# Kernel optimization log

Measured on AMD Instinct MI355X. Metric: run time of the kernel, lower is better.

## Reference

```python
import jax, jax.numpy as jnp
import numpy as np

I, H, L, B, T, EH = 256, 512, 2, 64, 2048, 128

def _leaky(x):
    return jnp.where(x > 0, x, 0.01 * x)

def _alpha(x):
    p = jax.nn.sigmoid(x)
    return p / (1.0 - p)

def _encoder(x, w1, b1, w2, b2, w3, b3):
    x = _leaky(x @ w1.T + b1)
    x = _leaky(x @ w2.T + b2)
    return _alpha(x @ w3.T + b3)

def setup_inputs() -> dict:
    key = jax.random.key(0)
    ks = jax.random.split(key, 24)
    def w(k, shape, fan_in):
        return jax.random.uniform(k, shape, jnp.float32, -1.0, 1.0) / np.sqrt(fan_in)
    inp = {
        "input": jax.random.normal(ks[0], (B, T, I), jnp.float32),
        "h0": jnp.zeros((L, B, H), jnp.float32),
        "c0": jnp.zeros((L, B, H), jnp.float32),
        # LSTM layer 0
        "W_ih0": w(ks[1], (4 * H, I), H), "W_hh0": w(ks[2], (4 * H, H), H),
        "b_ih0": w(ks[3], (4 * H,), H), "b_hh0": w(ks[4], (4 * H,), H),
        # LSTM layer 1
        "W_ih1": w(ks[5], (4 * H, H), H), "W_hh1": w(ks[6], (4 * H, H), H),
        "b_ih1": w(ks[7], (4 * H,), H), "b_hh1": w(ks[8], (4 * H,), H),
        # posterior_y encoder (input_size -> 128 -> 128 -> input_size)
        "ey_w1": w(ks[9], (EH, I), I), "ey_b1": w(ks[10], (EH,), I),
        "ey_w2": w(ks[11], (EH, EH), EH), "ey_b2": w(ks[12], (EH,), EH),
        "ey_w3": w(ks[13], (I, EH), EH), "ey_b3": w(ks[14], (I,), EH),
        # posterior_h encoder (hidden_size -> 128 -> 128 -> hidden_size)
        "eh_w1": w(ks[15], (EH, H), H), "eh_b1": w(ks[16], (EH,), H),
        "eh_w2": w(ks[17], (EH, EH), EH), "eh_b2": w(ks[18], (EH,), EH),
        "eh_w3": w(ks[19], (H, EH), EH), "eh_b3": w(ks[20], (H,), EH),
    }
    return inp

def reference(input, h0, c0,
              W_ih0, W_hh0, b_ih0, b_hh0,
              W_ih1, W_hh1, b_ih1, b_hh1,
              ey_w1, ey_b1, ey_w2, ey_b2, ey_w3, ey_b3,
              eh_w1, eh_b1, eh_w2, eh_b2, eh_w3, eh_b3):
    W_ih = [W_ih0, W_ih1]; W_hh = [W_hh0, W_hh1]
    b_ih = [b_ih0, b_ih1]; b_hh = [b_hh0, b_hh1]

    def step(carry, x_t):  # x_t: [B, I]
        h, c = carry  # each [L, B, H]
        alpha_y = _encoder(x_t, ey_w1, ey_b1, ey_w2, ey_b2, ey_w3, ey_b3)
        alpha_h = _encoder(h, eh_w1, eh_b1, eh_w2, eh_b2, eh_w3, eh_b3)
        h = h * alpha_h          # eval mode: noise = 1.0
        x = x_t * alpha_y
        new_h, new_c = [], []
        for l in range(L):
            gates = x @ W_ih[l].T + b_ih[l] + h[l] @ W_hh[l].T + b_hh[l]
            i, f, g, o = jnp.split(gates, 4, axis=-1)
            c_l = jax.nn.sigmoid(f) * c[l] + jax.nn.sigmoid(i) * jnp.tanh(g)
            h_l = jax.nn.sigmoid(o) * jnp.tanh(c_l)
            new_h.append(h_l); new_c.append(c_l)
            x = h_l
        return (jnp.stack(new_h), jnp.stack(new_c)), x  # x = top-layer h

    (h_n, c_n), ys = jax.lax.scan(step, (h0, c0), jnp.swapaxes(input, 0, 1))
    outputs = jnp.swapaxes(ys, 0, 1)  # [B, T, H]
    return outputs, h_n, c_n
```

## Files before the change

kernel.cpp:

```cpp
#include <hip/hip_runtime.h>
#include <math.h>
#include <stdint.h>

#define TT 2048
#define BB 64
#define II 256
#define HH 512
#define EHD 128
#define NGATE 64
#define NWG 68

typedef __attribute__((ext_vector_type(8))) short s16x8;
typedef __attribute__((ext_vector_type(4))) float f32x4;
typedef __attribute__((ext_vector_type(4))) uint32_t u32x4;

#define WAITVM(N) asm volatile("s_waitcnt vmcnt(" #N ")" ::: "memory")
#define VMFENCE() do { asm volatile("" ::: "memory"); __builtin_amdgcn_sched_barrier(0); } while(0)

__device__ __forceinline__ float dot4(const float4 a, const float4 b){
    return a.x*b.x + a.y*b.y + a.z*b.z + a.w*b.w;
}
__device__ __forceinline__ float sigm(float x){ return 1.0f/(1.0f+expf(-x)); }
__device__ __forceinline__ float leakyf(float x){ return x > 0.0f ? x : 0.01f*x; }
__device__ __forceinline__ float alphaf(float x){
    float p = 1.0f/(1.0f+expf(-x));
    return p/(1.0f-p);
}
__device__ __forceinline__ f32x4 MFMA(s16x8 a, s16x8 b, f32x4 c){
    return __builtin_amdgcn_mfma_f32_16x16x32_bf16(a, b, c, 0, 0, 0);
}

__device__ __forceinline__ uint32_t cld_u32(const uint32_t* p){
    return __hip_atomic_load(p, __ATOMIC_RELAXED, __HIP_MEMORY_SCOPE_AGENT);
}
__device__ __forceinline__ uint64_t cld_u64(const uint64_t* p){
    return __hip_atomic_load(p, __ATOMIC_RELAXED, __HIP_MEMORY_SCOPE_AGENT);
}
__device__ __forceinline__ void cst_u32(uint32_t* p, uint32_t v){
    __hip_atomic_store(p, v, __ATOMIC_RELAXED, __HIP_MEMORY_SCOPE_AGENT);
}

__device__ __forceinline__ uint32_t packsplit(float v){
    uint32_t u  = __float_as_uint(v);
    uint32_t hi = u & 0xFFFF0000u;
    float    lo = v - __uint_as_float(hi);
    return hi | (__float_as_uint(lo) >> 16);
}
__device__ __forceinline__ float unpackf(uint32_t w){
    return __uint_as_float(w & 0xFFFF0000u) + __uint_as_float(w << 16);
}

__device__ __forceinline__ void stage16(const void* g, void* l){
    __builtin_amdgcn_global_load_lds(
        (const __attribute__((address_space(1))) void*)g,
        (__attribute__((address_space(3))) void*)l, 16, 0, 0);
}

__device__ __forceinline__ void gbar(int* bar, int target){
    asm volatile("s_waitcnt vmcnt(0)" ::: "memory");
    __syncthreads();
    if (threadIdx.x == 0){
        __hip_atomic_fetch_add(bar, 1, __ATOMIC_RELAXED, __HIP_MEMORY_SCOPE_AGENT);
        while (__hip_atomic_load(bar, __ATOMIC_RELAXED, __HIP_MEMORY_SCOPE_AGENT) < target)
            __builtin_amdgcn_s_sleep(1);
    }
    __syncthreads();
}

__device__ __forceinline__ void wgbar(){ __builtin_amdgcn_s_barrier(); }
__device__ __forceinline__ void wgbar_lgkm(){
    asm volatile("s_waitcnt lgkmcnt(0)" ::: "memory");
    __builtin_amdgcn_s_barrier();
}

__device__ __forceinline__ void mk_frag(const uint64_t d[4], s16x8* hi, s16x8* lo){
    union { u32x4 u; s16x8 s; } H, L;
    #pragma unroll
    for (int i = 0; i < 4; i++){
        uint32_t x0 = (uint32_t)d[i], x1 = (uint32_t)(d[i] >> 32);
        H.u[i] = __builtin_amdgcn_perm(x1, x0, 0x07060302u);
        L.u[i] = __builtin_amdgcn_perm(x1, x0, 0x05040100u);
    }
    *hi = H.s; *lo = L.s;
}
__device__ __forceinline__ void pack8(const float* f, s16x8* hi, s16x8* lo){
    union { u32x4 u; s16x8 s; } H, L;
    #pragma unroll
    for (int i = 0; i < 4; i++){
        float a = f[2*i], b = f[2*i+1];
        uint32_t ua = __float_as_uint(a), ub = __float_as_uint(b);
        uint32_t ha = ua & 0xFFFF0000u, hb = ub & 0xFFFF0000u;
        H.u[i] = (ua >> 16) | hb;
        float la = a - __uint_as_float(ha), lb = b - __uint_as_float(hb);
        L.u[i] = (__float_as_uint(la) >> 16) | (__float_as_uint(lb) & 0xFFFF0000u);
    }
    *hi = H.s; *lo = L.s;
}

__device__ void enc_h_block(int e, const uint32_t* __restrict__ hsrc,
                            uint32_t* __restrict__ htil,
                            const float* __restrict__ w1, const float* __restrict__ b1,
                            const float* __restrict__ w2, const float* __restrict__ b2,
                            const float* __restrict__ w3, const float* __restrict__ b3,
                            float* smem)
{
    float* hlds = smem;
    float* t1   = smem + 4*516;
    float* t2   = t1 + 4*132;
    const int tid = threadIdx.x;
    const int r0 = e * 4;
    #pragma unroll
    for (int i = 0; i < 8; i++){
        int el = tid + i*256;
        int rr = el >> 9, k = el & 511;
        hlds[rr*516 + k] = unpackf(cld_u32(hsrc + (r0+rr)*HH + k));
    }
    __syncthreads();
    const int cc = tid & 63;
    const int rr = (tid >> 6) & 3;
    for (int cb = 0; cb < 2; cb++){
        int c = cc + cb*64;
        const float* wr = w1 + c*HH;
        const float* xr = hlds + rr*516;
        float a0 = b1[c], a1 = 0.f;
        #pragma unroll 8
        for (int k = 0; k < HH; k += 8){
            a0 += dot4(*(const float4*)(xr+k),   *(const float4*)(wr+k));
            a1 += dot4(*(const float4*)(xr+k+4), *(const float4*)(wr+k+4));
        }
        t1[rr*132 + c] = leakyf(a0 + a1);
    }
    __syncthreads();
    for (int cb = 0; cb < 2; cb++){
        int c = cc + cb*64;
        const float* wr = w2 + c*EHD;
        const float* xr = t1 + rr*132;
        float a0 = b2[c], a1 = 0.f;
        #pragma unroll 4
        for (int k = 0; k < EHD; k += 8){
            a0 += dot4(*(const float4*)(xr+k),   *(const float4*)(wr+k));
            a1 += dot4(*(const float4*)(xr+k+4), *(const float4*)(wr+k+4));
        }
        t2[rr*132 + c] = leakyf(a0 + a1);
    }
    __syncthreads();
    for (int cb = 0; cb < 8; cb++){
        int c = cc + cb*64;
        const float* wr = w3 + c*EHD;
        const float* xr = t2 + rr*132;
        float a0 = b3[c], a1 = 0.f;
        #pragma unroll 4
        for (int k = 0; k < EHD; k += 8){
            a0 += dot4(*(const float4*)(xr+k),   *(const float4*)(wr+k));
            a1 += dot4(*(const float4*)(xr+k+4), *(const float4*)(wr+k+4));
        }
        float a = alphaf(a0 + a1);
        cst_u32(htil + (r0+rr)*HH + c, packsplit(hlds[rr*516 + c] * a));
    }
    __syncthreads();
}

__global__ __launch_bounds__(256) void enc_only_kernel(
    const uint32_t* __restrict__ hsrc, uint32_t* __restrict__ htil,
    const float* __restrict__ w1, const float* __restrict__ b1,
    const float* __restrict__ w2, const float* __restrict__ b2,
    const float* __restrict__ w3, const float* __restrict__ b3)
{
    __shared__ float smem[3120];
    enc_h_block(blockIdx.x, hsrc, htil, w1, b1, w2, b2, w3, b3, smem);
}

__global__ __launch_bounds__(256) void ency_kernel(
    const float* __restrict__ xin, uint32_t* __restrict__ xprime,
    const float* __restrict__ w1, const float* __restrict__ b1,
    const float* __restrict__ w2, const float* __restrict__ b2,
    const float* __restrict__ w3, const float* __restrict__ b3)
{
    __shared__ float t1[32*128];
    __shared__ float t2[32*128];
    const long m0 = (long)blockIdx.x * 32;
    const int tid = threadIdx.x;
    const int cc = tid & 63;
    const int rr = tid >> 6;
    for (int cb = 0; cb < 2; cb++){
        int c = cc + cb*64;
        const float* wr = w1 + c*II;
        for (int q = 0; q < 8; q++){
            int r = rr*8 + q;
            const float* xr = xin + (m0 + r)*II;
            float a0 = b1[c], a1 = 0.f;
            #pragma unroll 8
            for (int k = 0; k < II; k += 8){
                a0 += dot4(*(const float4*)(xr+k),   *(const float4*)(wr+k));
                a1 += dot4(*(const float4*)(xr+k+4), *(const float4*)(wr+k+4));
            }
            t1[r*128 + c] = leakyf(a0 + a1);
        }
    }
    __syncthreads();
    for (int cb = 0; cb < 2; cb++){
        int c = cc + cb*64;
        const float* wr = w2 + c*EHD;
        for (int q = 0; q < 8; q++){
            int r = rr*8 + q;
            const float* xr = t1 + r*128;
            float a0 = b2[c], a1 = 0.f;
            #pragma unroll 4
            for (int k = 0; k < EHD; k += 8){
                a0 += dot4(*(const float4*)(xr+k),   *(const float4*)(wr+k));
                a1 += dot4(*(const float4*)(xr+k+4), *(const float4*)(wr+k+4));
            }
            t2[r*128 + c] = leakyf(a0 + a1);
        }
    }
    __syncthreads();
    for (int cb = 0; cb < 4; cb++){
        int c = cc + cb*64;
        const float* wr = w3 + c*EHD;
        for (int q = 0; q < 8; q++){
            int r = rr*8 + q;
            const float* xr = t2 + r*128;
            float a0 = b3[c], a1 = 0.f;
            #pragma unroll 4
            for (int k = 0; k < EHD; k += 8){
                a0 += dot4(*(const float4*)(xr+k),   *(const float4*)(wr+k));
                a1 += dot4(*(const float4*)(xr+k+4), *(const float4*)(wr+k+4));
            }
            float a = alphaf(a0 + a1);
            long m = m0 + r;
            long b = m >> 11, t = m & 2047;
            xprime[((long)t*BB + b)*II + c] = packsplit(xin[m*II + c] * a);
        }
    }
}

__global__ __launch_bounds__(64) void prep_pack_kernel(
    const float* __restrict__ Wih0, const float* __restrict__ Whh0,
    const float* __restrict__ Wih1, const float* __restrict__ Whh1,
    ushort* __restrict__ wpack)
{
    const int b = blockIdx.x;
    const int lane = threadIdx.x;
    const int g4 = b / 56, kts = b % 56;
    const int layer = (kts >= 24) ? 1 : 0;
    const int kt = layer ? (kts - 24) : kts;
    const int c = lane & 15;
    const int gate = c >> 2, uu = c & 3;
    const int n = gate*512 + g4*4 + uu;
    const int k = kt*32 + (lane >> 4)*8;
    const float* src;
    if (!layer){
        if (k < 256) src = Wih0 + (long)n*II + k;
        else         src = Whh0 + (long)n*HH + (k - 256);
    } else {
        if (k < 512) src = Wih1 + (long)n*HH + k;
        else         src = Whh1 + (long)n*HH + (k - 512);
    }
    ushort hi[8], lo[8];
    #pragma unroll
    for (int j = 0; j < 8; j++){
        float v = src[j];
        uint32_t u = __float_as_uint(v);
        hi[j] = (ushort)(u >> 16);
        float hf = __uint_as_float(u & 0xFFFF0000u);
        lo[j] = (ushort)(__float_as_uint(v - hf) >> 16);
    }
    long bhi = ((long)g4*7168 + kts*64 + lane) * 8;
    long blo = bhi + (long)3584*8;
    #pragma unroll
    for (int j = 0; j < 8; j++){ wpack[bhi + j] = hi[j]; wpack[blo + j] = lo[j]; }
}

__global__ __launch_bounds__(64) void enc_pack_kernel(
    const float* __restrict__ w1, const float* __restrict__ w2,
    const float* __restrict__ w3, ushort* __restrict__ epack)
{
    const int f = blockIdx.x;
    const int lane = threadIdx.x;
    const int c = lane & 15, kq = lane >> 4;
    const float* src;
    if (f < 128){
        int nt = f >> 4, kt = f & 15;
        src = w1 + (long)(nt*16 + c)*HH + kt*32 + kq*8;
    } else if (f < 160){
        int q = f - 128; int nt = q >> 2, kt = q & 3;
        src = w2 + (long)(nt*16 + c)*EHD + kt*32 + kq*8;
    } else {
        int q = f - 160; int nt = q >> 2, kt = q & 3;
        src = w3 + (long)(nt*16 + c)*EHD + kt*32 + kq*8;
    }
    long off = ((long)f*64 + lane)*8;
    #pragma unroll
    for (int j = 0; j < 8; j++){
        float v = src[j];
        uint32_t u = __float_as_uint(v);
        epack[off + j] = (ushort)(u >> 16);
        float hf = __uint_as_float(u & 0xFFFF0000u);
        epack[off + 147456 + j] = (ushort)(__float_as_uint(v - hf) >> 16);
    }
}

__global__ __launch_bounds__(256) void init_state_kernel(
    const float* __restrict__ h0, uint32_t* __restrict__ hpack, int* __restrict__ bar)
{
    int i = blockIdx.x*256 + threadIdx.x;
    hpack[i] = packsplit(h0[i]);
    if (i == 0) bar[0] = 0;
}

struct Accs { f32x4 a1, a2, b1, b2; };

template<int PHASE>
__device__ __forceinline__ void gate_aload(int c, int t, int brow, int kq,
    const uint32_t* __restrict__ xp, const uint32_t* __restrict__ h0p,
    const uint32_t* __restrict__ htilp, uint64_t* d)
{
    #pragma unroll
    for (int ktl = 0; ktl < 2; ktl++){
        const int kt = c*2 + ktl;
        const uint64_t* p;
        if (PHASE == 0){
            if (kt < 8) p = (const uint64_t*)(xp + ((long)t*BB + brow)*II) + kt*16 + kq*4;
            else        p = (const uint64_t*)(htilp + (long)brow*HH) + (kt-8)*16 + kq*4;
        } else {
            if (kt < 16) p = (const uint64_t*)(h0p + (long)brow*HH) + kt*16 + kq*4;
            else         p = (const uint64_t*)(htilp + (long)brow*HH) + (kt-16)*16 + kq*4;
        }
        #pragma unroll
        for (int i=0;i<4;i++) d[ktl*4+i] = cld_u64(p+i);
    }
}

template<int PHASE>
__device__ __forceinline__ void gate_phase(
    int t, int g, int tid,
    const s16x8* __restrict__ whl, char* __restrict__ wbuf,
    const s16x8* __restrict__ wlo0, const s16x8* __restrict__ wlo1,
    const uint32_t* __restrict__ xp,
    const uint32_t* __restrict__ h0p,
    const uint32_t* __restrict__ htilp,
    const float* bsum, uint32_t* __restrict__ hdst,
    float creg[2], float hreg[2], float* __restrict__ yout)
{
    const int lane = tid & 63;
    const int wv   = tid >> 6;
    const int brow = wv*16 + (lane & 15);
    const int kq   = lane >> 4;
    constexpr int NCH = PHASE ? 16 : 12;
    constexpr int KT0 = PHASE ? 24 : 0;

    const int sktl = wv >> 1, sng = wv & 1;
    const s16x8* swsrc = sng ? wlo1 : wlo0;
    const int sfi = sktl*2 + sng;

    Accs ac = {};
    uint64_t dA[2][8];

    stage16((const char*)(swsrc + (KT0 + 0 + sktl)*64) + lane*16, wbuf + 0*4096 + sfi*1024);
    VMFENCE();
    gate_aload<PHASE>(0, t, brow, kq, xp, h0p, htilp, dA[0]);
    VMFENCE();
    stage16((const char*)(swsrc + (KT0 + 2 + sktl)*64) + lane*16, wbuf + 1*4096 + sfi*1024);
    VMFENCE();
    gate_aload<PHASE>(1, t, brow, kq, xp, h0p, htilp, dA[1]);
    VMFENCE();

    #pragma unroll
    for (int c = 0; c < NCH; c++){
        if (c < NCH-1) { WAITVM(9); } else { WAITVM(0); }
        wgbar();
        s16x8 ah0, al0, ah1, al1;
        mk_frag(&dA[c&1][0], &ah0, &al0);
        mk_frag(&dA[c&1][4], &ah1, &al1);
        if (c + 2 < NCH){
            stage16((const char*)(swsrc + (KT0 + (c+2)*2 + sktl)*64) + lane*16,
                    wbuf + ((c+2)%3)*4096 + sfi*1024);
            VMFENCE();
            gate_aload<PHASE>(c+2, t, brow, kq, xp, h0p, htilp, dA[c&1]);
            VMFENCE();
        }
        const s16x8* sb = (const s16x8*)(wbuf + (c%3)*4096);
        #pragma unroll
        for (int ktl = 0; ktl < 2; ktl++){
            const int ktg = KT0 + c*2 + ktl;
            s16x8 ah = ktl ? ah1 : ah0;
            s16x8 al = ktl ? al1 : al0;
            { s16x8 B1 = whl[ktg*64 + lane];
              s16x8 B2 = sb[(ktl*2+0)*64 + lane];
              ac.a1 = MFMA(ah, B1, ac.a1);
              ac.a2 = MFMA(al, B1, ac.a2);
              ac.a2 = MFMA(ah, B2, ac.a2); }
            { s16x8 B1 = whl[3584 + ktg*64 + lane];
              s16x8 B2 = sb[(ktl*2+1)*64 + lane];
              ac.b1 = MFMA(ah, B1, ac.b1);
              ac.b2 = MFMA(al, B1, ac.b2);
              ac.b2 = MFMA(ah, B2, ac.b2); }
        }
    }
    wgbar_lgkm();
    float* glds = (float*)wbuf;
    {
        f32x4 caf = ac.a1 + ac.a2;
        f32x4 cbf = ac.b1 + ac.b2;
        const int r0 = wv*16 + (lane>>4)*4;
        const int c16 = lane & 15;
        #pragma unroll
        for (int i = 0; i < 4; i++){
            glds[(r0+i)*33 + c16]      = caf[i];
            glds[(r0+i)*33 + 16 + c16] = cbf[i];
        }
    }
    wgbar_lgkm();
    {
        const int jloc = tid & 7, bb2 = tid >> 3;
        const int ng = jloc >> 2, uu = jloc & 3;
        const int jcol = g*8 + jloc;
        #pragma unroll
        for (int half = 0; half < 2; half++){
            int b = bb2 + half*32;
            float gi = glds[b*33 + ng*16 + 0  + uu] + bsum[0];
            float gf = glds[b*33 + ng*16 + 4  + uu] + bsum[1];
            float gg = glds[b*33 + ng*16 + 8  + uu] + bsum[2];
            float go = glds[b*33 + ng*16 + 12 + uu] + bsum[3];
            float cn = sigm(gf)*creg[half] + sigm(gi)*tanhf(gg);
            float hn = sigm(go)*tanhf(cn);
            creg[half] = cn; hreg[half] = hn;
            cst_u32(hdst + b*HH + jcol, packsplit(hn));
            if (yout) yout[((long)b*TT + t)*HH + jcol] = hn;
        }
    }
}

__device__ __forceinline__ void enc_stage(int c, int wv, int lane,
                                          const char* __restrict__ epb, char* __restrict__ ebuf)
{
    char* slot = ebuf + (c%3)*8192;
    if (c < 8){
        #pragma unroll
        for (int ktl=0;ktl<2;ktl++)
        #pragma unroll
        for (int nt=0;nt<2;nt++)
        #pragma unroll
        for (int hl=0;hl<2;hl++){
            int f = (wv*2+nt)*16 + (c*2+ktl);
            long fidx = hl ? (288+f) : f;
            stage16(epb + fidx*1024 + lane*16, slot + (ktl*4+nt*2+hl)*1024);
        }
    } else if (c < 10){
        #pragma unroll
        for (int ktl=0;ktl<2;ktl++)
        #pragma unroll
        for (int nt=0;nt<2;nt++)
        #pragma unroll
        for (int hl=0;hl<2;hl++){
            int f = 128 + (wv*2+nt)*4 + ((c-8)*2+ktl);
            long fidx = hl ? (288+f) : f;
            stage16(epb + fidx*1024 + lane*16, slot + (ktl*4+nt*2+hl)*1024);
        }
    } else {
        int nt = c - 10;
        #pragma unroll
        for (int kt=0;kt<4;kt++)
        #pragma unroll
        for (int hl=0;hl<2;hl++){
            int f = 160 + (wv*8+nt)*4 + kt;
            long fidx = hl ? (288+f) : f;
            stage16(epb + fidx*1024 + lane*16, slot + (kt*2+hl)*1024);
        }
    }
}

__device__ void enc_phase(
    int e, const uint32_t* __restrict__ hsrc, uint32_t* __restrict__ htil,
    const char* __restrict__ epb, char* __restrict__ ebuf,
    const float bias1[2], const float bias2[2], const float bias3[8],
    float* __restrict__ t1, float* __restrict__ t2)
{
    const int tid = threadIdx.x;
    const int lane = tid & 63, wv = tid >> 6;
    const int c16 = lane & 15, kq = lane >> 4;
    const int r0 = e * 16;

    uint32_t hv[32];
    #pragma unroll
    for (int nt=0;nt<8;nt++)
      #pragma unroll
      for (int i=0;i<4;i++)
        hv[nt*4+i] = cld_u32(hsrc + (long)(r0+kq*4+i)*HH + wv*128 + nt*16 + c16);
    VMFENCE();

    const uint64_t* hp = (const uint64_t*)(hsrc + (long)(r0 + c16)*HH) + kq*4;
    uint64_t dA[32];
    #pragma unroll
    for (int kt=0;kt<8;kt++)
      #pragma unroll
      for (int i=0;i<4;i++)
        dA[kt*4+i] = cld_u64(hp + kt*16 + i);
    VMFENCE();

    enc_stage(0, wv, lane, epb, ebuf);
    VMFENCE();
    enc_stage(1, wv, lane, epb, ebuf);
    VMFENCE();
    WAITVM(16);
    s16x8 ah1[8], al1[8], ah2[8], al2[8];
    #pragma unroll
    for (int kt=0;kt<8;kt++) mk_frag(&dA[kt*4], &ah1[kt], &al1[kt]);
    #pragma unroll
    for (int kt=0;kt<8;kt++)
      #pragma unroll
      for (int i=0;i<4;i++)
        dA[kt*4+i] = cld_u64(hp + (kt+8)*16 + i);
    VMFENCE();

    f32x4 p1[2] = {{0,0,0,0},{0,0,0,0}};
    f32x4 p2[2] = {{0,0,0,0},{0,0,0,0}};
    #pragma unroll
    for (int c=0;c<8;c++){
        if (c < 2) { WAITVM(40); } else { WAITVM(8); }
        const s16x8* sb = (const s16x8*)(ebuf + (c%3)*8192);
        #pragma unroll
        for (int ktl=0;ktl<2;ktl++){
            const int kt = c*2 + ktl;
            s16x8 ah = (kt<8) ? ah1[kt&7] : ah2[kt&7];
            s16x8 al = (kt<8) ? al1[kt&7] : al2[kt&7];
            #pragma unroll
            for (int nt=0;nt<2;nt++){
                s16x8 bh = sb[(ktl*4+nt*2+0)*64 + lane];
                s16x8 bl = sb[(ktl*4+nt*2+1)*64 + lane];
                p1[nt] = MFMA(ah, bh, p1[nt]);
                p2[nt] = MFMA(al, bh, p2[nt]);
                p2[nt] = MFMA(ah, bl, p2[nt]);
            }
        }
        enc_stage(c+2, wv, lane, epb, ebuf);
        VMFENCE();
        if (c == 3){
            #pragma unroll
            for (int kt=0;kt<8;kt++) mk_frag(&dA[kt*4], &ah2[kt], &al2[kt]);
        }
    }
    #pragma unroll
    for (int nt=0;nt<2;nt++){
        f32x4 cc = p1[nt] + p2[nt];
        const int n = wv*32 + nt*16 + c16;
        #pragma unroll
        for (int i=0;i<4;i++) t1[(kq*4+i)*132 + n] = leakyf(cc[i] + bias1[nt]);
    }
    wgbar_lgkm();
    s16x8 a2h[4], a2l[4];
    #pragma unroll
    for (int kt=0;kt<4;kt++) pack8(t1 + c16*132 + kt*32 + kq*8, &a2h[kt], &a2l[kt]);
    f32x4 q1[2] = {{0,0,0,0},{0,0,0,0}};
    f32x4 q2[2] = {{0,0,0,0},{0,0,0,0}};
    #pragma unroll
    for (int c=8;c<10;c++){
        WAITVM(8);
        const s16x8* sb = (const s16x8*)(ebuf + (c%3)*8192);
        #pragma unroll
        for (int ktl=0;ktl<2;ktl++){
            const int kt = (c-8)*2 + ktl;
            #pragma unroll
            for (int nt=0;nt<2;nt++){
                s16x8 bh = sb[(ktl*4+nt*2+0)*64 + lane];
                s16x8 bl = sb[(ktl*4+nt*2+1)*64 + lane];
                q1[nt] = MFMA(a2h[kt], bh, q1[nt]);
                q2[nt] = MFMA(a2l[kt], bh, q2[nt]);
                q2[nt] = MFMA(a2h[kt], bl, q2[nt]);
            }
        }
        enc_stage(c+2, wv, lane, epb, ebuf);
        VMFENCE();
    }
    #pragma unroll
    for (int nt=0;nt<2;nt++){
        f32x4 cc = q1[nt] + q2[nt];
        const int n = wv*32 + nt*16 + c16;
        #pragma unroll
        for (int i=0;i<4;i++) t2[(kq*4+i)*132 + n] = leakyf(cc[i] + bias2[nt]);
    }
    wgbar_lgkm();
    s16x8 a3h[4], a3l[4];
    #pragma unroll
    for (int kt=0;kt<4;kt++) pack8(t2 + c16*132 + kt*32 + kq*8, &a3h[kt], &a3l[kt]);
    float av[8][4];
    #pragma unroll
    for (int c=10;c<18;c++){
        if (c < 17) { WAITVM(8); } else { WAITVM(0); }
        const int nt = c - 10;
        const s16x8* sb = (const s16x8*)(ebuf + (c%3)*8192);
        f32x4 s1 = {0,0,0,0}, s2 = {0,0,0,0};
        #pragma unroll
        for (int kt=0;kt<4;kt++){
            s16x8 bh = sb[(kt*2+0)*64 + lane];
            s16x8 bl = sb[(kt*2+1)*64 + lane];
            s1 = MFMA(a3h[kt], bh, s1);
            s2 = MFMA(a3l[kt], bh, s2);
            s2 = MFMA(a3h[kt], bl, s2);
        }
        f32x4 cc = s1 + s2;
        #pragma unroll
        for (int i=0;i<4;i++) av[nt][i] = alphaf(cc[i] + bias3[nt]);
        if (c + 2 < 18){
            enc_stage(c+2, wv, lane, epb, ebuf);
            VMFENCE();
        }
    }
    #pragma unroll
    for (int nt=0;nt<8;nt++)
      #pragma unroll
      for (int i=0;i<4;i++){
        const int row = r0 + kq*4 + i;
        const int n = wv*128 + nt*16 + c16;
        cst_u32(htil + (long)row*HH + n, packsplit(unpackf(hv[nt*4+i]) * av[nt][i]));
      }
}

__global__ __launch_bounds__(256, 1) void persistent_kernel(
    const uint32_t* __restrict__ xp,
    uint32_t* __restrict__ hpack,
    const ushort* __restrict__ wpack,
    const ushort* __restrict__ epack,
    const float* __restrict__ c0in,
    const float* __restrict__ bih0, const float* __restrict__ bhh0,
    const float* __restrict__ bih1, const float* __restrict__ bhh1,
    const float* __restrict__ ehb1, const float* __restrict__ ehb2,
    const float* __restrict__ ehb3,
    float* __restrict__ out, int* __restrict__ bar)
{
    extern __shared__ char smem_raw[];
    const int wg = blockIdx.x, tid = threadIdx.x;
    uint32_t* h0p = hpack;
    uint32_t* h1p = hpack + 32768;
    uint32_t* ht0 = hpack + 65536;
    uint32_t* ht1 = hpack + 98304;

    if (wg >= NGATE){
        char* ebuf = smem_raw + (tid>>6)*24576;
        float* t1 = (float*)(smem_raw + 98304);
        float* t2 = t1 + 16*132;
        const int e = wg - NGATE;
        const char* epb = (const char*)epack;
        const int lane = tid & 63, wv = tid >> 6, c16 = lane & 15;
        float bias1[2], bias2[2], bias3[8];
        #pragma unroll
        for (int nt = 0; nt < 2; nt++){
            bias1[nt] = ehb1[wv*32 + nt*16 + c16];
            bias2[nt] = ehb2[wv*32 + nt*16 + c16];
        }
        #pragma unroll
        for (int nt = 0; nt < 8; nt++)
            bias3[nt] = ehb3[wv*128 + nt*16 + c16];
        WAITVM(0);
        __syncthreads();
        for (int t = 0; t < TT; t++){
            enc_phase(e, h1p, ht1, epb, ebuf, bias1, bias2, bias3, t1, t2);
            gbar(bar, NWG*(2*t+1));
            enc_phase(e, h0p, ht0, epb, ebuf, bias1, bias2, bias3, t1, t2);
            gbar(bar, NWG*(2*t+2));
        }
        return;
    }
    s16x8* whl = (s16x8*)smem_raw;
    char*  wbuf = smem_raw + 114688;
    const int g = wg;
    const s16x8* wp = (const s16x8*)wpack;
    for (int i = tid; i < 7168; i += 256){
        int ng = (i >= 3584) ? 1 : 0;
        int r  = i - ng*3584;
        whl[i] = wp[(long)(2*g+ng)*7168 + r];
    }
    const s16x8* wlo0 = wp + (long)(2*g  )*7168 + 3584;
    const s16x8* wlo1 = wp + (long)(2*g+1)*7168 + 3584;

    const int jloc = tid & 7, bb2 = tid >> 3;
    const int jcol = g*8 + jloc;
    float bsum0[4], bsum1[4];
    #pragma unroll
    for (int q = 0; q < 4; q++){
        int n = q*512 + jcol;
        bsum0[q] = bih0[n] + bhh0[n];
        bsum1[q] = bih1[n] + bhh1[n];
    }
    float c0reg[2], c1reg[2], h0reg[2] = {0.f,0.f}, h1reg[2] = {0.f,0.f};
    #pragma unroll
    for (int half = 0; half < 2; half++){
        int b = bb2 + half*32;
        c0reg[half] = c0in[b*HH + jcol];
        c1reg[half] = c0in[32768 + b*HH + jcol];
    }
    WAITVM(0);
    __syncthreads();

    for (int t = 0; t < TT; t++){
        gate_phase<0>(t, g, tid, whl, wbuf, wlo0, wlo1,
                      xp, h0p, ht0, bsum0, h0p, c0reg, h0reg, nullptr);
        gbar(bar, NWG*(2*t+1));
        gate_phase<1>(t, g, tid, whl, wbuf, wlo0, wlo1,
                      xp, h0p, ht1, bsum1, h1p, c1reg, h1reg, out);
        gbar(bar, NWG*(2*t+2));
    }
    const long base = (long)BB*TT*HH;
    #pragma unroll
    for (int half = 0; half < 2; half++){
        int b = bb2 + half*32;
        out[base +                  b*HH + jcol] = h0reg[half];
        out[base + 32768          + b*HH + jcol] = h1reg[half];
        out[base + 65536          + b*HH + jcol] = c0reg[half];
        out[base + 65536 + 32768  + b*HH + jcol] = c1reg[half];
    }
}

extern "C" void kernel_launch(void* const* d_in, const int* in_sizes, int n_in,
                              void* d_out, int out_size, void* d_ws, size_t ws_size,
                              hipStream_t stream)
{
    const float* input = (const float*)d_in[0];
    const float* h0in  = (const float*)d_in[1];
    const float* c0in  = (const float*)d_in[2];
    const float* Wih0  = (const float*)d_in[3];
    const float* Whh0  = (const float*)d_in[4];
    const float* bih0  = (const float*)d_in[5];
    const float* bhh0  = (const float*)d_in[6];
    const float* Wih1  = (const float*)d_in[7];
    const float* Whh1  = (const float*)d_in[8];
    const float* bih1  = (const float*)d_in[9];
    const float* bhh1  = (const float*)d_in[10];
    const float* eyw1  = (const float*)d_in[11];
    const float* eyb1  = (const float*)d_in[12];
    const float* eyw2  = (const float*)d_in[13];
    const float* eyb2  = (const float*)d_in[14];
    const float* eyw3  = (const float*)d_in[15];
    const float* eyb3  = (const float*)d_in[16];
    const float* ehw1  = (const float*)d_in[17];
    const float* ehb1  = (const float*)d_in[18];
    const float* ehw2  = (const float*)d_in[19];
    const float* ehb2  = (const float*)d_in[20];
    const float* ehw3  = (const float*)d_in[21];
    const float* ehb3  = (const float*)d_in[22];

    float* out = (float*)d_out;
    float* ws  = (float*)d_ws;

    uint32_t* xprime = (uint32_t*)ws;
    uint32_t* hpack  = (uint32_t*)(ws + 33554432);
    int*      bar    = (int*)(ws + 33685504);
    ushort*   wpack  = (ushort*)(ws + 33751104);
    ushort*   epack  = (ushort*)(ws + 37421120);

    hipFuncSetAttribute((const void*)persistent_kernel,
                        hipFuncAttributeMaxDynamicSharedMemorySize, 131072);

    init_state_kernel<<<256, 256, 0, stream>>>(h0in, hpack, bar);
    prep_pack_kernel<<<128*56, 64, 0, stream>>>(Wih0, Whh0, Wih1, Whh1, wpack);
    enc_pack_kernel<<<288, 64, 0, stream>>>(ehw1, ehw2, ehw3, epack);
    ency_kernel<<<4096, 256, 0, stream>>>(input, xprime,
                                          eyw1, eyb1, eyw2, eyb2, eyw3, eyb3);
    enc_only_kernel<<<16, 256, 0, stream>>>(hpack, hpack + 65536,
                                            ehw1, ehb1, ehw2, ehb2, ehw3, ehb3);
    persistent_kernel<<<NWG, 256, 126976, stream>>>(
        xprime, hpack, wpack, epack, c0in,
        bih0, bhh0, bih1, bhh1,
        ehb1, ehb2, ehb3,
        out, bar);
}
```

Baseline: 92.95 ms.

## Split encoder workgroups per layer, shard barrier counter, deepen gate K-chunks

Encoder workgroups grow from four to eight. Each set handles one hidden layer and uses one-sided poll/arrive barriers, so encoders stop joining every grid-wide barrier. The single global barrier counter is split into eight padded slots, and pollers sum all eight, which spreads atomic contention. The gate phase now processes four K-tiles per pipeline chunk instead of two, with bigger LDS staging buffers, halving the number of workgroup barriers per phase. In exchange it uses more registers and LDS, and polling gets slower because each poll reads eight counters.

Result: slower. 118.6 ms (+27.6%).

```diff
diff --git a/kernel.cpp b/kernel.cpp
--- a/kernel.cpp
+++ b/kernel.cpp
@@ -8,7 +8,8 @@
 #define HH 512
 #define EHD 128
 #define NGATE 64
-#define NWG 68
+#define NWG 72
+#define ARRV 68
 
 typedef __attribute__((ext_vector_type(8))) short s16x8;
 typedef __attribute__((ext_vector_type(4))) float f32x4;
@@ -56,12 +57,35 @@
         (__attribute__((address_space(3))) void*)l, 16, 0, 0);
 }
 
+__device__ __forceinline__ int bar_sum(const int* bar){
+    int s = 0;
+    #pragma unroll
+    for (int i = 0; i < 8; i++)
+        s += (int)cld_u32((const uint32_t*)(bar + i*32));
+    return s;
+}
 __device__ __forceinline__ void gbar(int* bar, int target){
     asm volatile("s_waitcnt vmcnt(0)" ::: "memory");
     __syncthreads();
     if (threadIdx.x == 0){
-        __hip_atomic_fetch_add(bar, 1, __ATOMIC_RELAXED, __HIP_MEMORY_SCOPE_AGENT);
-        while (__hip_atomic_load(bar, __ATOMIC_RELAXED, __HIP_MEMORY_SCOPE_AGENT) < target)
+        __hip_atomic_fetch_add(bar + (blockIdx.x & 7)*32, 1,
+                               __ATOMIC_RELAXED, __HIP_MEMORY_SCOPE_AGENT);
+        while (bar_sum(bar) < target)
+            __builtin_amdgcn_s_sleep(1);
+    }
+    __syncthreads();
+}
+__device__ __forceinline__ void gbar_arrive(int* bar){
+    asm volatile("s_waitcnt vmcnt(0)" ::: "memory");
+    __syncthreads();
+    if (threadIdx.x == 0)
+        __hip_atomic_fetch_add(bar + (blockIdx.x & 7)*32, 1,
+                               __ATOMIC_RELAXED, __HIP_MEMORY_SCOPE_AGENT);
+    __syncthreads();
+}
+__device__ __forceinline__ void gbar_poll(const int* bar, int target){
+    if (threadIdx.x == 0){
+        while (bar_sum(bar) < target)
             __builtin_amdgcn_s_sleep(1);
     }
     __syncthreads();
@@ -305,19 +329,19 @@
 {
     int i = blockIdx.x*256 + threadIdx.x;
     hpack[i] = packsplit(h0[i]);
-    if (i == 0) bar[0] = 0;
+    if (blockIdx.x == 0 && threadIdx.x < 256) bar[threadIdx.x] = 0;
 }
 
 struct Accs { f32x4 a1, a2, b1, b2; };
 
 template<int PHASE>
-__device__ __forceinline__ void gate_aload(int c, int t, int brow, int kq,
+__device__ __forceinline__ void gate_aload4(int c, int t, int brow, int kq,
     const uint32_t* __restrict__ xp, const uint32_t* __restrict__ h0p,
     const uint32_t* __restrict__ htilp, uint64_t* d)
 {
     #pragma unroll
-    for (int ktl = 0; ktl < 2; ktl++){
-        const int kt = c*2 + ktl;
+    for (int ktl = 0; ktl < 4; ktl++){
+        const int kt = c*4 + ktl;
         const uint64_t* p;
         if (PHASE == 0){
             if (kt < 8) p = (const uint64_t*)(xp + ((long)t*BB + brow)*II) + kt*16 + kq*4;
@@ -329,6 +353,16 @@
         #pragma unroll
         for (int i=0;i<4;i++) d[ktl*4+i] = cld_u64(p+i);
     }
+}
+
+__device__ __forceinline__ void gate_stage4(int c, int wv, int lane, int KT0,
+    const s16x8* __restrict__ wlo0, const s16x8* __restrict__ wlo1,
+    char* __restrict__ wbuf)
+{
+    char* slot = wbuf + (c%3)*8192;
+    const int ktg = KT0 + c*4 + wv;
+    stage16((const char*)(wlo0 + (long)ktg*64) + lane*16, slot + (wv*2+0)*1024);
+    stage16((const char*)(wlo1 + (long)ktg*64) + lane*16, slot + (wv*2+1)*1024);
 }
 
 template<int PHASE>
@@ -346,55 +380,49 @@
     const int wv   = tid >> 6;
     const int brow = wv*16 + (lane & 15);
     const int kq   = lane >> 4;
-    constexpr int NCH = PHASE ? 16 : 12;
+    constexpr int NCH = PHASE ? 8 : 6;
     constexpr int KT0 = PHASE ? 24 : 0;
 
-    const int sktl = wv >> 1, sng = wv & 1;
-    const s16x8* swsrc = sng ? wlo1 : wlo0;
-    const int sfi = sktl*2 + sng;
-
     Accs ac = {};
-    uint64_t dA[2][8];
-
-    stage16((const char*)(swsrc + (KT0 + 0 + sktl)*64) + lane*16, wbuf + 0*4096 + sfi*1024);
+    uint64_t dA[2][16];
+
+    gate_stage4(0, wv, lane, KT0, wlo0, wlo1, wbuf);
     VMFENCE();
-    gate_aload<PHASE>(0, t, brow, kq, xp, h0p, htilp, dA[0]);
+    gate_aload4<PHASE>(0, t, brow, kq, xp, h0p, htilp, dA[0]);
     VMFENCE();
-    stage16((const char*)(swsrc + (KT0 + 2 + sktl)*64) + lane*16, wbuf + 1*4096 + sfi*1024);
+    gate_stage4(1, wv, lane, KT0, wlo0, wlo1, wbuf);
     VMFENCE();
-    gate_aload<PHASE>(1, t, brow, kq, xp, h0p, htilp, dA[1]);
+    gate_aload4<PHASE>(1, t, brow, kq, xp, h0p, htilp, dA[1]);
     VMFENCE();
 
     #pragma unroll
     for (int c = 0; c < NCH; c++){
-        if (c < NCH-1) { WAITVM(9); } else { WAITVM(0); }
+        if (c < NCH-1) { WAITVM(18); } else { WAITVM(0); }
         wgbar();
-        s16x8 ah0, al0, ah1, al1;
-        mk_frag(&dA[c&1][0], &ah0, &al0);
-        mk_frag(&dA[c&1][4], &ah1, &al1);
+        s16x8 ah[4], al[4];
+        #pragma unroll
+        for (int ktl = 0; ktl < 4; ktl++)
+            mk_frag(&dA[c&1][ktl*4], &ah[ktl], &al[ktl]);
         if (c + 2 < NCH){
-            stage16((const char*)(swsrc + (KT0 + (c+2)*2 + sktl)*64) + lane*16,
-                    wbuf + ((c+2)%3)*4096 + sfi*1024);
+            gate_stage4(c+2, wv, lane, KT0, wlo0, wlo1, wbuf);
             VMFENCE();
-            gate_aload<PHASE>(c+2, t, brow, kq, xp, h0p, htilp, dA[c&1]);
+            gate_aload4<PHASE>(c+2, t, brow, kq, xp, h0p, htilp, dA[c&1]);
             VMFENCE();
         }
-        const s16x8* sb = (const s16x8*)(wbuf + (c%3)*4096);
-        #pragma unroll
-        for (int ktl = 0; ktl < 2; ktl++){
-            const int ktg = KT0 + c*2 + ktl;
-            s16x8 ah = ktl ? ah1 : ah0;
-            s16x8 al = ktl ? al1 : al0;
+        const s16x8* sb = (const s16x8*)(wbuf + (c%3)*8192);
+        #pragma unroll
+        for (int ktl = 0; ktl < 4; ktl++){
+            const int ktg = KT0 + c*4 + ktl;
             { s16x8 B1 = whl[ktg*64 + lane];
               s16x8 B2 = sb[(ktl*2+0)*64 + lane];
-              ac.a1 = MFMA(ah, B1, ac.a1);
-              ac.a2 = MFMA(al, B1, ac.a2);
-              ac.a2 = MFMA(ah, B2, ac.a2); }
+              ac.a1 = MFMA(ah[ktl], B1, ac.a1);
+              ac.a2 = MFMA(al[ktl], B1, ac.a2);
+              ac.a2 = MFMA(ah[ktl], B2, ac.a2); }
             { s16x8 B1 = whl[3584 + ktg*64 + lane];
               s16x8 B2 = sb[(ktl*2+1)*64 + lane];
-              ac.b1 = MFMA(ah, B1, ac.b1);
-              ac.b2 = MFMA(al, B1, ac.b2);
-              ac.b2 = MFMA(ah, B2, ac.b2); }
+              ac.b1 = MFMA(ah[ktl], B1, ac.b1);
+              ac.b2 = MFMA(al[ktl], B1, ac.b2);
+              ac.b2 = MFMA(ah[ktl], B2, ac.b2); }
         }
     }
     wgbar_lgkm();
@@ -639,7 +667,8 @@
         char* ebuf = smem_raw + (tid>>6)*24576;
         float* t1 = (float*)(smem_raw + 98304);
         float* t2 = t1 + 16*132;
-        const int e = wg - NGATE;
+        const bool is_h1 = (wg < NGATE + 4);
+        const int e = (wg - NGATE) & 3;
         const char* epb = (const char*)epack;
         const int lane = tid & 63, wv = tid >> 6, c16 = lane & 15;
         float bias1[2], bias2[2], bias3[8];
@@ -653,11 +682,18 @@
             bias3[nt] = ehb3[wv*128 + nt*16 + c16];
         WAITVM(0);
         __syncthreads();
-        for (int t = 0; t < TT; t++){
-            enc_phase(e, h1p, ht1, epb, ebuf, bias1, bias2, bias3, t1, t2);
-            gbar(bar, NWG*(2*t+1));
-            enc_phase(e, h0p, ht0, epb, ebuf, bias1, bias2, bias3, t1, t2);
-            gbar(bar, NWG*(2*t+2));
+        if (is_h1){
+            for (int t = 0; t < TT; t++){
+                gbar_poll(bar, ARRV*(2*t));
+                enc_phase(e, h1p, ht1, epb, ebuf, bias1, bias2, bias3, t1, t2);
+                gbar_arrive(bar);
+            }
+        } else {
+            for (int t = 0; t < TT; t++){
+                gbar_poll(bar, ARRV*(2*t+1));
+                enc_phase(e, h0p, ht0, epb, ebuf, bias1, bias2, bias3, t1, t2);
+                gbar_arrive(bar);
+            }
         }
         return;
     }
@@ -695,10 +731,10 @@
     for (int t = 0; t < TT; t++){
         gate_phase<0>(t, g, tid, whl, wbuf, wlo0, wlo1,
                       xp, h0p, ht0, bsum0, h0p, c0reg, h0reg, nullptr);
-        gbar(bar, NWG*(2*t+1));
+        gbar(bar, ARRV*(2*t+1));
         gate_phase<1>(t, g, tid, whl, wbuf, wlo0, wlo1,
                       xp, h0p, ht1, bsum1, h1p, c1reg, h1reg, out);
-        gbar(bar, NWG*(2*t+2));
+        gbar(bar, ARRV*(2*t+2));
     }
     const long base = (long)BB*TT*HH;
     #pragma unroll
@@ -749,7 +785,7 @@
     ushort*   epack  = (ushort*)(ws + 37421120);
 
     hipFuncSetAttribute((const void*)persistent_kernel,
-                        hipFuncAttributeMaxDynamicSharedMemorySize, 131072);
+                        hipFuncAttributeMaxDynamicSharedMemorySize, 139264);
 
     init_state_kernel<<<256, 256, 0, stream>>>(h0in, hpack, bar);
     prep_pack_kernel<<<128*56, 64, 0, stream>>>(Wih0, Whh0, Wih1, Whh1, wpack);
@@ -758,7 +794,7 @@
                                           eyw1, eyb1, eyw2, eyb2, eyw3, eyb3);
     enc_only_kernel<<<16, 256, 0, stream>>>(hpack, hpack + 65536,
                                             ehw1, ehb1, ehw2, ehb2, ehw3, ehb3);
-    persistent_kernel<<<NWG, 256, 126976, stream>>>(
+    persistent_kernel<<<NWG, 256, 139264, stream>>>(
         xprime, hpack, wpack, epack, c0in,
         bih0, bhh0, bih1, bhh1,
         ehb1, ehb2, ehb3,
```

## Shard grid barrier counters and use a master-broadcast epoch flag

Applied to the files above, without the earlier changes.

Replaces the single global atomic counter barrier with 8 counters spread across separate cache lines, each block incrementing one by blockIdx. Block 0 alone polls the sum of the counters and then publishes an epoch flag, which all other blocks poll. This is meant to cut atomic contention and polling traffic on one address across 68 workgroups, 4096 barriers in total. In exchange, every barrier gains an extra hop through the master block, and correctness depends on cld/cst being coherent loads and stores.

New measurement: 93.89 ms. Within noise of the previous version (+1.0%).

```diff
diff --git a/kernel.cpp b/kernel.cpp
--- a/kernel.cpp
+++ b/kernel.cpp
@@ -56,13 +56,28 @@
         (__attribute__((address_space(3))) void*)l, 16, 0, 0);
 }
 
-__device__ __forceinline__ void gbar(int* bar, int target){
+__device__ __forceinline__ int bar_sum(const int* bar){
+    int s = 0;
+    #pragma unroll
+    for (int i = 0; i < 8; i++)
+        s += (int)cld_u32((const uint32_t*)(bar + i*32));
+    return s;
+}
+__device__ __forceinline__ void gbar(int* bar, int epoch){
     asm volatile("s_waitcnt vmcnt(0)" ::: "memory");
     __syncthreads();
     if (threadIdx.x == 0){
-        __hip_atomic_fetch_add(bar, 1, __ATOMIC_RELAXED, __HIP_MEMORY_SCOPE_AGENT);
-        while (__hip_atomic_load(bar, __ATOMIC_RELAXED, __HIP_MEMORY_SCOPE_AGENT) < target)
-            __builtin_amdgcn_s_sleep(1);
+        __hip_atomic_fetch_add(bar + (blockIdx.x & 7)*32, 1,
+                               __ATOMIC_RELAXED, __HIP_MEMORY_SCOPE_AGENT);
+        if (blockIdx.x == 0){
+            const int target = NWG * epoch;
+            while (bar_sum(bar) < target)
+                __builtin_amdgcn_s_sleep(1);
+            cst_u32((uint32_t*)(bar + 8*32), (uint32_t)epoch);
+        } else {
+            while ((int)cld_u32((const uint32_t*)(bar + 8*32)) < epoch)
+                __builtin_amdgcn_s_sleep(2);
+        }
     }
     __syncthreads();
 }
@@ -305,7 +320,7 @@
 {
     int i = blockIdx.x*256 + threadIdx.x;
     hpack[i] = packsplit(h0[i]);
-    if (i == 0) bar[0] = 0;
+    if (i < 320) bar[i] = 0;
 }
 
 struct Accs { f32x4 a1, a2, b1, b2; };
@@ -655,9 +670,9 @@
         __syncthreads();
         for (int t = 0; t < TT; t++){
             enc_phase(e, h1p, ht1, epb, ebuf, bias1, bias2, bias3, t1, t2);
-            gbar(bar, NWG*(2*t+1));
+            gbar(bar, 2*t+1);
             enc_phase(e, h0p, ht0, epb, ebuf, bias1, bias2, bias3, t1, t2);
-            gbar(bar, NWG*(2*t+2));
+            gbar(bar, 2*t+2);
         }
         return;
     }
@@ -695,10 +710,10 @@
     for (int t = 0; t < TT; t++){
         gate_phase<0>(t, g, tid, whl, wbuf, wlo0, wlo1,
                       xp, h0p, ht0, bsum0, h0p, c0reg, h0reg, nullptr);
-        gbar(bar, NWG*(2*t+1));
+        gbar(bar, 2*t+1);
         gate_phase<1>(t, g, tid, whl, wbuf, wlo0, wlo1,
                       xp, h0p, ht1, bsum1, h1p, c1reg, h1reg, out);
-        gbar(bar, NWG*(2*t+2));
+        gbar(bar, 2*t+2);
     }
     const long base = (long)BB*TT*HH;
     #pragma unroll
```
